# Kernel optimization log

Measured on AMD Instinct MI355X. Metric: run time of the kernel, lower is better.

The kernel has to match this reference:

```python
import jax, jax.numpy as jnp
import numpy as np

NORM_EPS = 1e-6   # config.norm_eps
MAG_EPS = 1e-6    # config.magnitude_eps


def setup_inputs() -> dict:
    key = jax.random.key(0)
    k0, k1, k2, k3, k4, k5 = jax.random.split(key, 6)
    B, S, IN, OUT, R, L = 4, 2048, 2048, 2048, 4, 16
    x = jax.random.normal(k0, (B, S, IN), dtype=jnp.float32)
    # frozen quantization indices (buffer _indices), values in [0, lut_size)
    indices = jax.random.randint(k1, (OUT, IN), 0, L, dtype=jnp.int32)
    # monotonic LUT in [-1, 1] (make_lut with include_zero=False)
    lut = jnp.linspace(-1.0, 1.0, L, dtype=jnp.float32)
    scale_A = jax.random.normal(k2, (OUT, R), dtype=jnp.float32)
    scale_B = jax.random.normal(k3, (R, IN), dtype=jnp.float32)
    rank_magnitude = jax.random.uniform(k4, (R,), dtype=jnp.float32)
    bias = jax.random.normal(k5, (OUT,), dtype=jnp.float32) * 0.01
    return {"x": x, "indices": indices, "lut": lut, "scale_A": scale_A,
            "scale_B": scale_B, "rank_magnitude": rank_magnitude, "bias": bias}


def reference(x, indices, lut, scale_A, scale_B, rank_magnitude, bias):
    # _get_normalized_scales: force_positive_scales='abs', magnitude_activation='softplus'
    A = jnp.abs(scale_A)                                            # [out, r]
    A_dir = A / jnp.maximum(jnp.linalg.norm(A, axis=0, keepdims=True), NORM_EPS)
    Bm = jnp.abs(scale_B)                                           # [r, in]
    B_dir = Bm / jnp.maximum(jnp.linalg.norm(Bm, axis=1, keepdims=True), NORM_EPS)
    g = jax.nn.softplus(rank_magnitude) + MAG_EPS                   # [r]
    # LUT dequant: Q = lut[_indices], [out, in]
    Q = lut[indices]
    # rank-by-rank forward: y = sum_k g_k * (a_k \odot (Q (b_k \odot x))) + bias
    # t[b,s,r,o] = sum_i x[b,s,i] * B_dir[r,i] * Q[o,i]
    t = jnp.einsum('bsi,ri,oi->bsro', x, B_dir, Q)
    y = jnp.einsum('bsro,or,r->bso', t, A_dir, g) + bias
    return y
```

## Files before the change

kernel.cpp:

```cpp
#include <hip/hip_runtime.h>

#define IN_DIM  2048
#define OUT_DIM 2048
#define MROWS   8192
#define RANK    4
#define BK      64

typedef unsigned short ushort_t;
typedef __attribute__((ext_vector_type(8))) short  short8;
typedef __attribute__((ext_vector_type(4))) float  floatx4;

__device__ __forceinline__ unsigned short f2bf(float f) {
  union { float f; unsigned int u; } v; v.f = f;
  unsigned int r = v.u + 0x7fffu + ((v.u >> 16) & 1u);
  return (unsigned short)(r >> 16);
}

__device__ __forceinline__ void gload16(const ushort_t* g, short* l) {
  __builtin_amdgcn_global_load_lds(
      (const __attribute__((address_space(1))) void*)g,
      (__attribute__((address_space(3))) void*)l, 16, 0, 0);
}

__global__ void coef_kernel(const float* __restrict__ sA, const float* __restrict__ sB,
                            const float* __restrict__ mag, float* __restrict__ cOut) {
  __shared__ float part[8][256];
  __shared__ float tot[8];
  int t = threadIdx.x;
  float sa[4] = {0.f, 0.f, 0.f, 0.f};
  for (int o = t; o < OUT_DIM; o += 256) {
    float4 v = *(const float4*)(sA + o * 4);
    sa[0] += v.x * v.x; sa[1] += v.y * v.y; sa[2] += v.z * v.z; sa[3] += v.w * v.w;
  }
  float sb[4] = {0.f, 0.f, 0.f, 0.f};
  for (int r = 0; r < 4; ++r)
    for (int i = t; i < IN_DIM; i += 256) { float v = sB[r * IN_DIM + i]; sb[r] += v * v; }
  for (int q = 0; q < 4; ++q) { part[q][t] = sa[q]; part[4 + q][t] = sb[q]; }
  __syncthreads();
  if (t < 8) { float s = 0.f; for (int j = 0; j < 256; ++j) s += part[t][j]; tot[t] = s; }
  __syncthreads();
  if (t < 4) {
    float g  = log1pf(expf(mag[t])) + 1e-6f;
    float na = fmaxf(sqrtf(tot[t]),     1e-6f);
    float nb = fmaxf(sqrtf(tot[4 + t]), 1e-6f);
    cOut[t] = g / (na * nb);
  }
}

__global__ void prep_kernel(const float* __restrict__ x, ushort_t* __restrict__ xb,
                            const int* __restrict__ idx, const float* __restrict__ lut,
                            const float* __restrict__ sA, const float* __restrict__ sB,
                            const float* __restrict__ c, ushort_t* __restrict__ W) {
  int t = threadIdx.x;
  if (blockIdx.x < 8192) {
    size_t i = ((size_t)blockIdx.x * 256 + t) * 8;
    float4 a = *(const float4*)(x + i);
    float4 b = *(const float4*)(x + i + 4);
    uint4 o4;
    o4.x = (unsigned)f2bf(a.x) | ((unsigned)f2bf(a.y) << 16);
    o4.y = (unsigned)f2bf(a.z) | ((unsigned)f2bf(a.w) << 16);
    o4.z = (unsigned)f2bf(b.x) | ((unsigned)f2bf(b.y) << 16);
    o4.w = (unsigned)f2bf(b.z) | ((unsigned)f2bf(b.w) << 16);
    *(uint4*)(xb + i) = o4;
  } else {
    __shared__ float aA[4];
    __shared__ float lutS[16];
    int o = blockIdx.x - 8192;
    if (t < 4)  aA[t]   = fabsf(sA[o * 4 + t]) * c[t];
    if (t < 16) lutS[t] = lut[t];
    __syncthreads();
    int i = t * 8;
    const int4* ip4 = (const int4*)(idx + (size_t)o * IN_DIM + i);
    int4 i0 = ip4[0], i1 = ip4[1];
    int ii[8] = {i0.x, i0.y, i0.z, i0.w, i1.x, i1.y, i1.z, i1.w};
    unsigned short u[8];
    #pragma unroll
    for (int j = 0; j < 8; ++j) {
      float s = aA[0] * fabsf(sB[0 * IN_DIM + i + j])
              + aA[1] * fabsf(sB[1 * IN_DIM + i + j])
              + aA[2] * fabsf(sB[2 * IN_DIM + i + j])
              + aA[3] * fabsf(sB[3 * IN_DIM + i + j]);
      u[j] = f2bf(lutS[ii[j]] * s);
    }
    uint4 o4;
    o4.x = (unsigned)u[0] | ((unsigned)u[1] << 16);
    o4.y = (unsigned)u[2] | ((unsigned)u[3] << 16);
    o4.z = (unsigned)u[4] | ((unsigned)u[5] << 16);
    o4.w = (unsigned)u[6] | ((unsigned)u[7] << 16);
    *(uint4*)(W + (size_t)o * IN_DIM + i) = o4;
  }
}


#define MFMA16(a, b, c) __builtin_amdgcn_mfma_f32_16x16x32_bf16(a, b, c, 0, 0, 0)

__device__ __forceinline__ void stage_half(const ushort_t* gbase, short* ldsbase,
                                           int tile, int h, int wid) {
  gload16(gbase + (size_t)h * 64 * IN_DIM + (size_t)tile * BK,
          ldsbase + (h * 512 + wid * 64) * 8);
  gload16(gbase + ((size_t)h * 64 + 128) * IN_DIM + (size_t)tile * BK,
          ldsbase + (1024 + h * 512 + wid * 64) * 8);
}

template <int MQ, bool FIRST, typename StageFn>
__device__ __forceinline__ void phase(const short* aRd, const short* bRd,
                                      int ko0, int ko1,
                                      floatx4 (&acc)[8][4],
                                      short8 (&bf0)[4], short8 (&bf1)[4],
                                      StageFn&& stage, int vm) {
  if (FIRST) {
    #pragma unroll
    for (int ni = 0; ni < 4; ++ni) {
      bf0[ni] = *(const short8*)(bRd + ni * 1024 + ko0);
      bf1[ni] = *(const short8*)(bRd + ni * 1024 + ko1);
    }
  }
  short8 a0k0 = *(const short8*)(aRd + (2 * MQ) * 1024 + ko0);
  short8 a0k1 = *(const short8*)(aRd + (2 * MQ) * 1024 + ko1);
  short8 a1k0 = *(const short8*)(aRd + (2 * MQ + 1) * 1024 + ko0);
  short8 a1k1 = *(const short8*)(aRd + (2 * MQ + 1) * 1024 + ko1);
  stage();
  if (FIRST)        asm volatile("s_waitcnt lgkmcnt(8)");
  if (vm == 6)      asm volatile("s_waitcnt vmcnt(6)");
  else if (vm == 0) asm volatile("s_waitcnt vmcnt(0)");
  __builtin_amdgcn_s_barrier();
  __builtin_amdgcn_s_setprio(1);
  #pragma unroll
  for (int ni = 0; ni < 4; ++ni) {
    acc[2 * MQ    ][ni] = MFMA16(a0k0, bf0[ni], acc[2 * MQ    ][ni]);
    acc[2 * MQ    ][ni] = MFMA16(a0k1, bf1[ni], acc[2 * MQ    ][ni]);
    acc[2 * MQ + 1][ni] = MFMA16(a1k0, bf0[ni], acc[2 * MQ + 1][ni]);
    acc[2 * MQ + 1][ni] = MFMA16(a1k1, bf1[ni], acc[2 * MQ + 1][ni]);
  }
  __builtin_amdgcn_s_setprio(0);
  __builtin_amdgcn_s_barrier();
}

__global__ __launch_bounds__(512, 2) void gemm_kernel(const ushort_t* __restrict__ A,
                                                      const ushort_t* __restrict__ W,
                                                      const float* __restrict__ bias,
                                                      float* __restrict__ C) {
  __shared__ short lA0[16384];
  __shared__ short lB0[16384];
  __shared__ short lA1[16384];
  __shared__ short lB1[16384];

  const int t    = threadIdx.x;
  const int lane = t & 63;
  const int wid  = t >> 6;
  const int wr   = wid >> 2;
  const int wc   = wid & 3;

  const int flat  = blockIdx.y * 8 + blockIdx.x;
  const int xcd   = flat & 7;
  const int slot  = flat >> 3;
  const int tileY = (xcd >> 1) * 8 + (slot >> 2);
  const int tileX = (xcd & 1) * 4 + (slot & 3);
  const int rowBase = tileY * 256;
  const int colBase = tileX * 256;

  const int srcRow   = wid * 8 + (lane >> 3);
  const int srcChunk = (lane & 7) ^ (lane >> 3);
  const ushort_t* gA = A + (size_t)(rowBase + srcRow) * IN_DIM + srcChunk * 8;
  const ushort_t* gB = W + (size_t)(colBase + srcRow) * IN_DIM + srcChunk * 8;

  const int rA  = lane & 15;
  const int kh  = lane >> 4;
  const int sw  = rA & 7;
  const int ko0 = ((kh)     ^ sw) * 8;
  const int ko1 = ((4 + kh) ^ sw) * 8;
  const short* aRd0 = lA0 + (wr * 128 + rA) * 64;
  const short* bRd0 = lB0 + (wc * 64  + rA) * 64;
  const short* aRd1 = lA1 + (wr * 128 + rA) * 64;
  const short* bRd1 = lB1 + (wc * 64  + rA) * 64;

  floatx4 acc[8][4];
  #pragma unroll
  for (int i = 0; i < 8; ++i)
    #pragma unroll
    for (int j = 0; j < 4; ++j) acc[i][j] = (floatx4){0.f, 0.f, 0.f, 0.f};
  short8 bf0[4], bf1[4];

  stage_half(gA, lA0, 0, 0, wid);
  stage_half(gA, lA0, 0, 1, wid);
  stage_half(gB, lB0, 0, 0, wid);
  stage_half(gB, lB0, 0, 1, wid);
  stage_half(gB, lB1, 1, 0, wid);
  stage_half(gB, lB1, 1, 1, wid);
  stage_half(gA, lA1, 1, 0, wid);
  asm volatile("s_waitcnt vmcnt(6)");
  __builtin_amdgcn_s_barrier();

  #pragma unroll 1
  for (int i = 0; i < 16; ++i) {
    const int  t2   = 2 * i + 2, t3 = 2 * i + 3;
    const bool more = (i < 15);
    phase<0, true >(aRd0, bRd0, ko0, ko1, acc, bf0, bf1,
                    [&] { stage_half(gA, lA1, 2 * i + 1, 1, wid); }, -1);
    phase<1, false>(aRd0, bRd0, ko0, ko1, acc, bf0, bf1,
                    [&] { if (more) stage_half(gB, lB0, t2, 0, wid); }, -1);
    phase<2, false>(aRd0, bRd0, ko0, ko1, acc, bf0, bf1,
                    [&] { if (more) stage_half(gB, lB0, t2, 1, wid); }, -1);
    phase<3, false>(aRd0, bRd0, ko0, ko1, acc, bf0, bf1,
                    [&] { if (more) stage_half(gA, lA0, t2, 0, wid); }, more ? 6 : 0);
    phase<0, true >(aRd1, bRd1, ko0, ko1, acc, bf0, bf1,
                    [&] { if (more) stage_half(gA, lA0, t2, 1, wid); }, -1);
    phase<1, false>(aRd1, bRd1, ko0, ko1, acc, bf0, bf1,
                    [&] { if (more) stage_half(gB, lB1, t3, 0, wid); }, -1);
    phase<2, false>(aRd1, bRd1, ko0, ko1, acc, bf0, bf1,
                    [&] { if (more) stage_half(gB, lB1, t3, 1, wid); }, -1);
    phase<3, false>(aRd1, bRd1, ko0, ko1, acc, bf0, bf1,
                    [&] { if (more) stage_half(gA, lA1, t3, 0, wid); }, more ? 6 : -1);
  }

  const int mB = rowBase + wr * 128 + (lane >> 4) * 4;
  const int nB = colBase + wc * 64 + (lane & 15);
  #pragma unroll
  for (int ni = 0; ni < 4; ++ni) {
    float bv = bias[nB + ni * 16];
    #pragma unroll
    for (int mi = 0; mi < 8; ++mi)
      #pragma unroll
      for (int r = 0; r < 4; ++r)
        C[(size_t)(mB + mi * 16 + r) * OUT_DIM + (nB + ni * 16)] = acc[mi][ni][r] + bv;
  }
}

extern "C" void kernel_launch(void* const* d_in, const int* in_sizes, int n_in,
                              void* d_out, int out_size, void* d_ws, size_t ws_size,
                              hipStream_t stream) {
  const float* x    = (const float*)d_in[0];
  const int*   idx  = (const int*)d_in[1];
  const float* lut  = (const float*)d_in[2];
  const float* sA   = (const float*)d_in[3];
  const float* sB   = (const float*)d_in[4];
  const float* mag  = (const float*)d_in[5];
  const float* bias = (const float*)d_in[6];
  float* y = (float*)d_out;

  char* ws = (char*)d_ws;
  float*    c  = (float*)ws;
  ushort_t* W  = (ushort_t*)(ws + 256);
  ushort_t* xb = (ushort_t*)(ws + 256 + (size_t)OUT_DIM * IN_DIM * 2);

  coef_kernel<<<1, 256, 0, stream>>>(sA, sB, mag, c);
  prep_kernel<<<8192 + OUT_DIM, 256, 0, stream>>>(x, xb, idx, lut, sA, sB, c, W);
  dim3 g(OUT_DIM / 256, MROWS / 256);
  gemm_kernel<<<g, 512, 0, stream>>>(xb, W, bias, y);
}
```

Baseline: 220.4 us.

## Prefetch next phase's A fragments from LDS into double-buffered registers

Each GEMM phase now loads the A-operand LDS fragments for the following phase into a second register set right after the barrier. The current phase's MFMAs use fragments loaded one phase earlier, so LDS read latency is meant to overlap with matrix math instead of stalling before each MFMA block. B fragment loads move after the barrier, and a sched_barrier stops the compiler from reordering the loads. The extra fragment registers raise VGPR pressure under the 512x2 launch bounds, which could cause spills or lower occupancy.

```diff
diff --git a/kernel.cpp b/kernel.cpp
--- a/kernel.cpp
+++ b/kernel.cpp
@@ -102,35 +102,40 @@
           ldsbase + (1024 + h * 512 + wid * 64) * 8);
 }
 
-template <int MQ, bool FIRST, typename StageFn>
-__device__ __forceinline__ void phase(const short* aRd, const short* bRd,
+template <int MQ, int NMQ, bool FIRST, typename StageFn>
+__device__ __forceinline__ void phase(const short* bRd, const short* aNextBase,
                                       int ko0, int ko1,
+                                      short8 (&aCur)[4], short8 (&aNext)[4],
+                                      short8 (&bf)[8],
                                       floatx4 (&acc)[8][4],
-                                      short8 (&bf0)[4], short8 (&bf1)[4],
                                       StageFn&& stage, int vm) {
-  if (FIRST) {
-    #pragma unroll
-    for (int ni = 0; ni < 4; ++ni) {
-      bf0[ni] = *(const short8*)(bRd + ni * 1024 + ko0);
-      bf1[ni] = *(const short8*)(bRd + ni * 1024 + ko1);
-    }
-  }
-  short8 a0k0 = *(const short8*)(aRd + (2 * MQ) * 1024 + ko0);
-  short8 a0k1 = *(const short8*)(aRd + (2 * MQ) * 1024 + ko1);
-  short8 a1k0 = *(const short8*)(aRd + (2 * MQ + 1) * 1024 + ko0);
-  short8 a1k1 = *(const short8*)(aRd + (2 * MQ + 1) * 1024 + ko1);
   stage();
-  if (FIRST)        asm volatile("s_waitcnt lgkmcnt(8)");
   if (vm == 6)      asm volatile("s_waitcnt vmcnt(6)");
   else if (vm == 0) asm volatile("s_waitcnt vmcnt(0)");
   __builtin_amdgcn_s_barrier();
+  if (FIRST) {
+    #pragma unroll
+    for (int ni = 0; ni < 4; ++ni) {
+      bf[ni]     = *(const short8*)(bRd + ni * 1024 + ko0);
+      bf[4 + ni] = *(const short8*)(bRd + ni * 1024 + ko1);
+    }
+  }
+  {
+    const short* p0 = aNextBase + (2 * NMQ) * 1024;
+    const short* p1 = aNextBase + (2 * NMQ + 1) * 1024;
+    aNext[0] = *(const short8*)(p0 + ko0);
+    aNext[1] = *(const short8*)(p0 + ko1);
+    aNext[2] = *(const short8*)(p1 + ko0);
+    aNext[3] = *(const short8*)(p1 + ko1);
+  }
+  __builtin_amdgcn_sched_barrier(0);
   __builtin_amdgcn_s_setprio(1);
   #pragma unroll
   for (int ni = 0; ni < 4; ++ni) {
-    acc[2 * MQ    ][ni] = MFMA16(a0k0, bf0[ni], acc[2 * MQ    ][ni]);
-    acc[2 * MQ    ][ni] = MFMA16(a0k1, bf1[ni], acc[2 * MQ    ][ni]);
-    acc[2 * MQ + 1][ni] = MFMA16(a1k0, bf0[ni], acc[2 * MQ + 1][ni]);
-    acc[2 * MQ + 1][ni] = MFMA16(a1k1, bf1[ni], acc[2 * MQ + 1][ni]);
+    acc[2 * MQ    ][ni] = MFMA16(aCur[0], bf[ni],     acc[2 * MQ    ][ni]);
+    acc[2 * MQ    ][ni] = MFMA16(aCur[1], bf[4 + ni], acc[2 * MQ    ][ni]);
+    acc[2 * MQ + 1][ni] = MFMA16(aCur[2], bf[ni],     acc[2 * MQ + 1][ni]);
+    acc[2 * MQ + 1][ni] = MFMA16(aCur[3], bf[4 + ni], acc[2 * MQ + 1][ni]);
   }
   __builtin_amdgcn_s_setprio(0);
   __builtin_amdgcn_s_barrier();
@@ -179,7 +184,7 @@
   for (int i = 0; i < 8; ++i)
     #pragma unroll
     for (int j = 0; j < 4; ++j) acc[i][j] = (floatx4){0.f, 0.f, 0.f, 0.f};
-  short8 bf0[4], bf1[4];
+  short8 aX[4], aY[4], bf[8];
 
   stage_half(gA, lA0, 0, 0, wid);
   stage_half(gA, lA0, 0, 1, wid);
@@ -191,26 +196,31 @@
   asm volatile("s_waitcnt vmcnt(6)");
   __builtin_amdgcn_s_barrier();
 
+  aX[0] = *(const short8*)(aRd0 + 0 * 1024 + ko0);
+  aX[1] = *(const short8*)(aRd0 + 0 * 1024 + ko1);
+  aX[2] = *(const short8*)(aRd0 + 1 * 1024 + ko0);
+  aX[3] = *(const short8*)(aRd0 + 1 * 1024 + ko1);
+
   #pragma unroll 1
   for (int i = 0; i < 16; ++i) {
     const int  t2   = 2 * i + 2, t3 = 2 * i + 3;
     const bool more = (i < 15);
-    phase<0, true >(aRd0, bRd0, ko0, ko1, acc, bf0, bf1,
-                    [&] { stage_half(gA, lA1, 2 * i + 1, 1, wid); }, -1);
-    phase<1, false>(aRd0, bRd0, ko0, ko1, acc, bf0, bf1,
-                    [&] { if (more) stage_half(gB, lB0, t2, 0, wid); }, -1);
-    phase<2, false>(aRd0, bRd0, ko0, ko1, acc, bf0, bf1,
-                    [&] { if (more) stage_half(gB, lB0, t2, 1, wid); }, -1);
-    phase<3, false>(aRd0, bRd0, ko0, ko1, acc, bf0, bf1,
-                    [&] { if (more) stage_half(gA, lA0, t2, 0, wid); }, more ? 6 : 0);
-    phase<0, true >(aRd1, bRd1, ko0, ko1, acc, bf0, bf1,
-                    [&] { if (more) stage_half(gA, lA0, t2, 1, wid); }, -1);
-    phase<1, false>(aRd1, bRd1, ko0, ko1, acc, bf0, bf1,
-                    [&] { if (more) stage_half(gB, lB1, t3, 0, wid); }, -1);
-    phase<2, false>(aRd1, bRd1, ko0, ko1, acc, bf0, bf1,
-                    [&] { if (more) stage_half(gB, lB1, t3, 1, wid); }, -1);
-    phase<3, false>(aRd1, bRd1, ko0, ko1, acc, bf0, bf1,
-                    [&] { if (more) stage_half(gA, lA1, t3, 0, wid); }, more ? 6 : -1);
+    phase<0, 1, true >(bRd0, aRd0, ko0, ko1, aX, aY, bf, acc,
+                       [&] { stage_half(gA, lA1, 2 * i + 1, 1, wid); }, -1);
+    phase<1, 2, false>(bRd0, aRd0, ko0, ko1, aY, aX, bf, acc,
+                       [&] { if (more) stage_half(gB, lB0, t2, 0, wid); }, -1);
+    phase<2, 3, false>(bRd0, aRd0, ko0, ko1, aX, aY, bf, acc,
+                       [&] { if (more) stage_half(gB, lB0, t2, 1, wid); }, -1);
+    phase<3, 0, false>(bRd0, aRd1, ko0, ko1, aY, aX, bf, acc,
+                       [&] { if (more) stage_half(gA, lA0, t2, 0, wid); }, more ? 6 : 0);
+    phase<0, 1, true >(bRd1, aRd1, ko0, ko1, aX, aY, bf, acc,
+                       [&] { if (more) stage_half(gA, lA0, t2, 1, wid); }, -1);
+    phase<1, 2, false>(bRd1, aRd1, ko0, ko1, aY, aX, bf, acc,
+                       [&] { if (more) stage_half(gB, lB1, t3, 0, wid); }, -1);
+    phase<2, 3, false>(bRd1, aRd1, ko0, ko1, aX, aY, bf, acc,
+                       [&] { if (more) stage_half(gB, lB1, t3, 1, wid); }, -1);
+    phase<3, 0, false>(bRd1, aRd0, ko0, ko1, aY, aX, bf, acc,
+                       [&] { if (more) stage_half(gA, lA1, t3, 0, wid); }, more ? 6 : -1);
   }
 
   const int mB = rowBase + wr * 128 + (lane >> 4) * 4;
```

Measured after the change: 219.6 us. Within noise of the previous version (-0.4%).
